# Kernel optimization log

Measured on AMD Instinct MI355X. Metric: run time of the kernel, lower is better.

## Reference

```python
import jax, jax.numpy as jnp
import numpy as np

NEG_INF = -1e9  # mask fill value used by the original layer
LEAKY_SLOPE = 0.2


def setup_inputs() -> dict:
    key = jax.random.key(0)
    k1, k2, k3, k4 = jax.random.split(key, 4)
    B, N, D_in = 8, 1024, 256
    H, head_dim = 8, 32  # output_dim=256, concat_heads=True
    node_features = jax.random.normal(k1, (B, N, D_in), dtype=jnp.float32)
    adjacency = jax.random.randint(k2, (B, N, N), 0, 2, dtype=jnp.int32)
    W = jax.random.normal(k3, (H, D_in, head_dim), dtype=jnp.float32) * (1.0 / np.sqrt(D_in))
    a = jax.random.normal(k4, (H, 2 * head_dim), dtype=jnp.float32) * (1.0 / np.sqrt(2 * head_dim))
    bias = jnp.zeros((H * head_dim,), dtype=jnp.float32)
    return {"node_features": node_features, "adjacency": adjacency, "W": W, "a": a, "bias": bias}


def reference(node_features, adjacency, W, a, bias):
    # node_features: (B,N,D_in); adjacency: (B,N,N) in {0,1}
    H, _, hd = W.shape
    # Per-head linear transform: (B,H,N,head_dim)
    Wh = jnp.einsum('bni,hij->bhnj', node_features, W)
    # a @ concat(h_i, h_j) == a1 @ h_i + a2 @ h_j  (avoids O(N^2*2hd) concat)
    a1, a2 = a[:, :hd], a[:, hd:]
    e_i = jnp.einsum('bhnj,hj->bhn', Wh, a1)  # (B,H,N) source term
    e_j = jnp.einsum('bhnj,hj->bhn', Wh, a2)  # (B,H,N) target term
    scores = e_i[:, :, :, None] + e_j[:, :, None, :]  # (B,H,N,N)
    # LeakyReLU(0.2) exactly as ops.maximum(x, 0.2*x)
    scores = jnp.maximum(scores, LEAKY_SLOPE * scores)
    mask = adjacency.astype(scores.dtype)[:, None, :, :]  # (B,1,N,N)
    masked = scores * mask + (1.0 - mask) * NEG_INF
    attn = jax.nn.softmax(masked, axis=-1)  # (B,H,N,N)
    attended = jnp.einsum('bhij,bhjk->bhik', attn, Wh)  # (B,H,N,hd)
    B, _, N, _ = attended.shape
    # concat heads -> (B,N,H*hd); head order matches the python loop concat
    out = attended.transpose(0, 2, 1, 3).reshape(B, N, H * hd)
    out = out + bias
    return jax.nn.relu(out)
```

## Files before the change

kernel.cpp:

```cpp
#include <hip/hip_runtime.h>

#define GAT_B   8
#define GAT_N   1024
#define GAT_DIN 256
#define GAT_H   8
#define GAT_HD  32
#define GAT_LOG2E 1.4426950408889634f

typedef unsigned short gu16;
typedef unsigned int   gu32;
typedef unsigned long long gu64;
typedef __bf16 bf16x8 __attribute__((ext_vector_type(8)));
typedef __bf16 bf16x4 __attribute__((ext_vector_type(4)));
typedef float  f32x4v __attribute__((ext_vector_type(4)));

#if __has_builtin(__builtin_amdgcn_exp2f)
#define GAT_EXP2(x) __builtin_amdgcn_exp2f(x)
#else
#define GAT_EXP2(x) exp2f(x)
#endif

__device__ __forceinline__ float gb2f(gu16 u) { return __uint_as_float(((gu32)u) << 16); }

__device__ __forceinline__ void gat_detect(const gu16* p, int t, int* sflag) {
    if (t < 64) {
        int e0 = (p[2 * t]     >> 7) & 0xFF;
        int e1 = (p[2 * t + 1] >> 7) & 0xFF;
        unsigned long long m = __ballot((e0 >= 140) || (e1 >= 140));
        if (t == 0) *sflag = (m != 0ULL);
    }
}

__global__ __launch_bounds__(512) void CustomGATLayer_90348932038855_pack(
    const void* __restrict__ Xv, const int* __restrict__ adj, const void* __restrict__ Wv,
    gu64* __restrict__ pk, __bf16* __restrict__ wfg)
{
    __shared__ int sflag;
    const int t = threadIdx.x, bid = blockIdx.x;
    gat_detect((const gu16*)Xv, t, &sflag);
    __syncthreads();
    const int fp32 = sflag;

    if (bid < 8) {
        const int h = bid;
        if (fp32) {
            const float* ws = (const float*)Wv + (size_t)h * 8192;
            #pragma unroll
            for (int q = 0; q < 4; ++q) {
                int idx = q * 2048 + t * 4;
                int i = idx >> 5, k = idx & 31;
                float4 v = *(const float4*)(ws + idx);
                int d = h * 8192 + (((i >> 5) * 32 + k) * 4 + ((i >> 3) & 3)) * 8 + (i & 7);
                wfg[d] = (__bf16)v.x; wfg[d + 32] = (__bf16)v.y;
                wfg[d + 64] = (__bf16)v.z; wfg[d + 96] = (__bf16)v.w;
            }
        } else {
            const gu16* ws = (const gu16*)Wv + (size_t)h * 8192;
            gu16* wo = (gu16*)wfg;
            #pragma unroll
            for (int q = 0; q < 4; ++q) {
                int idx = q * 2048 + t * 4;
                int i = idx >> 5, k = idx & 31;
                ushort4 v = *(const ushort4*)(ws + idx);
                int d = h * 8192 + (((i >> 5) * 32 + k) * 4 + ((i >> 3) & 3)) * 8 + (i & 7);
                wo[d] = v.x; wo[d + 32] = v.y; wo[d + 64] = v.z; wo[d + 96] = v.w;
            }
        }
    }

    const int w = t >> 6, l = t & 63;
    const int r0 = bid * 32 + w * 4;
    for (int r = 0; r < 4; ++r) {
        const int* ar = adj + (size_t)(r0 + r) * GAT_N;
        gu64* po = pk + (size_t)(r0 + r) * 16;
        #pragma unroll
        for (int s = 0; s < 16; ++s) {
            int v = ar[s * 64 + l];
            gu64 m = __ballot(v != 0);
            if (l == 0) po[s] = m;
        }
    }
}

__global__ __launch_bounds__(512) void CustomGATLayer_90348932038855_kernel(
    const void* __restrict__ Xv, const __bf16* __restrict__ wfg, const void* __restrict__ Av,
    __bf16* __restrict__ whb, float* __restrict__ e1, float* __restrict__ e2)
{
    __shared__ __align__(16) __bf16 Xl[16][264];
    __shared__ int sflag;

    const int t = threadIdx.x;
    gat_detect((const gu16*)Xv, t, &sflag);

    const int bt = blockIdx.x;
    const int M0 = bt * 16, b = M0 >> 10, nloc = M0 & 1023;
    const int srow = t >> 5, scol = (t & 31) * 8;
    __syncthreads();
    const int fp32 = sflag;

    if (fp32) {
        const float* xs = (const float*)Xv + ((size_t)(b * GAT_N + nloc + srow)) * GAT_DIN + scol;
        float4 x0 = *(const float4*)(xs);
        float4 x1 = *(const float4*)(xs + 4);
        bf16x8 xv;
        xv[0] = (__bf16)x0.x; xv[1] = (__bf16)x0.y; xv[2] = (__bf16)x0.z; xv[3] = (__bf16)x0.w;
        xv[4] = (__bf16)x1.x; xv[5] = (__bf16)x1.y; xv[6] = (__bf16)x1.z; xv[7] = (__bf16)x1.w;
        *(bf16x8*)&Xl[srow][scol] = xv;
    } else {
        const gu16* xs = (const gu16*)Xv + ((size_t)(b * GAT_N + nloc + srow)) * GAT_DIN + scol;
        *(bf16x8*)&Xl[srow][scol] = *(const bf16x8*)xs;
    }
    __syncthreads();

    const int h = t >> 6, l = t & 63, g = l >> 4, c = l & 15;
    const __bf16* wf = wfg + h * 8192;

    f32x4v acc0 = {0.f, 0.f, 0.f, 0.f};
    f32x4v acc1 = {0.f, 0.f, 0.f, 0.f};
    #pragma unroll
    for (int kc = 0; kc < 8; ++kc) {
        bf16x8 af = *(const bf16x8*)&Xl[c][kc * 32 + 8 * g];
        bf16x8 b0 = *(const bf16x8*)(wf + ((kc * 32 + c) * 4 + g) * 8);
        bf16x8 b1 = *(const bf16x8*)(wf + ((kc * 32 + c + 16) * 4 + g) * 8);
        acc0 = __builtin_amdgcn_mfma_f32_16x16x32_bf16(af, b0, acc0, 0, 0, 0);
        acc1 = __builtin_amdgcn_mfma_f32_16x16x32_bf16(af, b1, acc1, 0, 0, 0);
    }

    const int nb = nloc + 4 * g;
    const int jcc = nb >> 5, kg = (nb >> 3) & 3, e0 = nb & 7;
    const size_t fb = (((size_t)(b * GAT_H + h) * 32 + jcc) * 4 + kg) * 32;
    bf16x4 v0, v1;
    v0[0] = (__bf16)acc0[0]; v0[1] = (__bf16)acc0[1];
    v0[2] = (__bf16)acc0[2]; v0[3] = (__bf16)acc0[3];
    v1[0] = (__bf16)acc1[0]; v1[1] = (__bf16)acc1[1];
    v1[2] = (__bf16)acc1[2]; v1[3] = (__bf16)acc1[3];
    *(bf16x4*)(whb + (fb + c) * 8 + e0)      = v0;
    *(bf16x4*)(whb + (fb + c + 16) * 8 + e0) = v1;

    float a1c, a1c16, a2c, a2c16;
    if (fp32) {
        const float* ap = (const float*)Av + h * 2 * GAT_HD;
        a1c = ap[c] * GAT_LOG2E;      a1c16 = ap[c + 16] * GAT_LOG2E;
        a2c = ap[32 + c] * GAT_LOG2E; a2c16 = ap[48 + c] * GAT_LOG2E;
    } else {
        const gu16* ap = (const gu16*)Av + h * 2 * GAT_HD;
        a1c = gb2f(ap[c]) * GAT_LOG2E;      a1c16 = gb2f(ap[c + 16]) * GAT_LOG2E;
        a2c = gb2f(ap[32 + c]) * GAT_LOG2E; a2c16 = gb2f(ap[48 + c]) * GAT_LOG2E;
    }
    float p1[4], p2[4];
    #pragma unroll
    for (int q = 0; q < 4; ++q) {
        p1[q] = acc0[q] * a1c + acc1[q] * a1c16;
        p2[q] = acc0[q] * a2c + acc1[q] * a2c16;
        #pragma unroll
        for (int mm = 1; mm <= 8; mm <<= 1) {
            p1[q] += __shfl_xor(p1[q], mm);
            p2[q] += __shfl_xor(p2[q], mm);
        }
    }
    if (c == 0) {
        const size_t eb = (size_t)(b * GAT_H + h) * GAT_N + nb;
        #pragma unroll
        for (int q = 0; q < 4; ++q) { e1[eb + q] = p1[q]; e2[eb + q] = p2[q]; }
    }
}

__global__ __launch_bounds__(512) void CustomGATLayer_90348932038855_attn(
    const void* __restrict__ Xv, const gu32* __restrict__ pk32, const void* __restrict__ biasv,
    const __bf16* __restrict__ whb, const float* __restrict__ e1f, const float* __restrict__ e2f,
    float* __restrict__ out)
{
    __shared__ __align__(16) float e2l[GAT_H * GAT_N];
    __shared__ gu32 pkl[16][33];
    __shared__ int sflag;

    const int t = threadIdx.x;
    const int h = t >> 6, l = t & 63, g = l >> 4, c = l & 15;
    const int id = blockIdx.x;
    const int b = id & 7, tile = id >> 3;
    const int i0 = tile * 16;

    gat_detect((const gu16*)Xv, t, &sflag);

    {
        const int prow = t >> 5, pjc = t & 31;
        pkl[prow][pjc] = pk32[((size_t)(b * GAT_N + i0 + prow)) * 32 + pjc];
    }
    {
        const float* s = e2f + (size_t)(b * GAT_H + h) * GAT_N;
        float* d = e2l + h * GAT_N;
        #pragma unroll
        for (int q = 0; q < 4; ++q) {
            int off = (q * 64 + l) * 4;
            *(float4*)(d + off) = *(const float4*)(s + off);
        }
    }
    __syncthreads();
    const int fp32 = sflag;

    const float e1r = e1f[(size_t)(b * GAT_H + h) * GAT_N + i0 + c];
    const __bf16* whr = whb + (size_t)(b * GAT_H + h) * (GAT_N * GAT_HD) + g * 256 + c * 8;
    const float* e2h = e2l + h * GAT_N + 8 * g;

    bf16x8 wA0 = *(const bf16x8*)(whr),        wA1 = *(const bf16x8*)(whr + 128);
    bf16x8 wB0 = *(const bf16x8*)(whr + 1024), wB1 = *(const bf16x8*)(whr + 1152);

    f32x4v acc0 = {0.f, 0.f, 0.f, 0.f};
    f32x4v acc1 = {0.f, 0.f, 0.f, 0.f};
    f32x4v accS = {0.f, 0.f, 0.f, 0.f};
    bf16x8 onesf;
    #pragma unroll
    for (int e = 0; e < 8; ++e) onesf[e] = (__bf16)1.0f;

#define GAT_WCOMP(EV, IDX) {                        \
        float s_ = e1r + (EV);                      \
        s_ = fmaxf(s_, 0.2f * s_);                  \
        s_ = fminf(s_, 86.0f);                      \
        float w_ = GAT_EXP2(s_);                    \
        w_ = (ab & (1u << IDX)) ? w_ : 0.0f;        \
        pf[IDX] = (__bf16)w_; }

    #pragma unroll 2
    for (int jc = 0; jc < 32; ++jc) {
        const bf16x8 w0 = wA0, w1 = wA1;
        wA0 = wB0; wA1 = wB1;
        if (jc < 30) {
            const __bf16* wn = whr + (jc + 2) * 1024;
            wB0 = *(const bf16x8*)wn; wB1 = *(const bf16x8*)(wn + 128);
        }
        const gu32 ab = (pkl[c][jc] >> (8 * g)) & 0xFFu;
        float4 ea = *(const float4*)(e2h + jc * 32);
        float4 eb = *(const float4*)(e2h + jc * 32 + 4);
        bf16x8 pf;
        GAT_WCOMP(ea.x, 0) GAT_WCOMP(ea.y, 1)
        GAT_WCOMP(ea.z, 2) GAT_WCOMP(ea.w, 3)
        GAT_WCOMP(eb.x, 4) GAT_WCOMP(eb.y, 5)
        GAT_WCOMP(eb.z, 6) GAT_WCOMP(eb.w, 7)
        acc0 = __builtin_amdgcn_mfma_f32_16x16x32_bf16(pf, w0, acc0, 0, 0, 0);
        acc1 = __builtin_amdgcn_mfma_f32_16x16x32_bf16(pf, w1, acc1, 0, 0, 0);
        accS = __builtin_amdgcn_mfma_f32_16x16x32_bf16(pf, onesf, accS, 0, 0, 0);
    }
#undef GAT_WCOMP

    float bv0, bv1;
    if (fp32) {
        const float* bp = (const float*)biasv + h * GAT_HD;
        bv0 = bp[c]; bv1 = bp[c + 16];
    } else {
        const gu16* bp = (const gu16*)biasv + h * GAT_HD;
        bv0 = gb2f(bp[c]); bv1 = gb2f(bp[c + 16]);
    }

    float* ob = out + (size_t)(b * GAT_N + i0) * (GAT_H * GAT_HD) + h * GAT_HD + c;
    #pragma unroll
    for (int q = 0; q < 4; ++q) {
        float d = accS[q];
        float r = (d > 0.f) ? (1.0f / d) : 0.0f;
        float o0 = fmaxf(acc0[q] * r + bv0, 0.f);
        float o1 = fmaxf(acc1[q] * r + bv1, 0.f);
        ob[(size_t)(4 * g + q) * (GAT_H * GAT_HD)]      = o0;
        ob[(size_t)(4 * g + q) * (GAT_H * GAT_HD) + 16] = o1;
    }
}

extern "C" void kernel_launch(void* const* d_in, const int* in_sizes, int n_in,
                              void* d_out, int out_size, void* d_ws, size_t ws_size,
                              hipStream_t stream) {
    const void* X    = d_in[0];
    const int*  adj  = (const int*)d_in[1];
    const void* Wm   = d_in[2];
    const void* Av   = d_in[3];
    const void* bias = d_in[4];
    float* outp = (float*)d_out;

    __bf16* whb = (__bf16*)d_ws;
    float* e1  = (float*)(whb + (size_t)GAT_B * GAT_H * GAT_N * GAT_HD);
    float* e2  = e1 + (size_t)GAT_B * GAT_H * GAT_N;
    __bf16* wfg = (__bf16*)(e2 + (size_t)GAT_B * GAT_H * GAT_N);
    gu64* pk   = (gu64*)(wfg + (size_t)GAT_H * GAT_DIN * GAT_HD);

    CustomGATLayer_90348932038855_pack
        <<<dim3(256), 512, 0, stream>>>(X, adj, Wm, pk, wfg);
    CustomGATLayer_90348932038855_kernel
        <<<dim3(512), 512, 0, stream>>>(X, wfg, Av, whb, e1, e2);
    CustomGATLayer_90348932038855_attn
        <<<dim3((GAT_N / 16) * GAT_B), 512, 0, stream>>>(
            X, (const gu32*)pk, bias, whb, e1, e2, outp);
}
```

Measured before the change: 135.6 us.

## Fuse adjacency bit-packing into attention kernel and deepen Wh prefetch

```diff
diff --git a/kernel.cpp b/kernel.cpp
--- a/kernel.cpp
+++ b/kernel.cpp
@@ -9,7 +9,6 @@
 
 typedef unsigned short gu16;
 typedef unsigned int   gu32;
-typedef unsigned long long gu64;
 typedef __bf16 bf16x8 __attribute__((ext_vector_type(8)));
 typedef __bf16 bf16x4 __attribute__((ext_vector_type(4)));
 typedef float  f32x4v __attribute__((ext_vector_type(4)));
@@ -32,52 +31,35 @@
 }
 
 __global__ __launch_bounds__(512) void CustomGATLayer_90348932038855_pack(
-    const void* __restrict__ Xv, const int* __restrict__ adj, const void* __restrict__ Wv,
-    gu64* __restrict__ pk, __bf16* __restrict__ wfg)
+    const void* __restrict__ Xv, const void* __restrict__ Wv, __bf16* __restrict__ wfg)
 {
     __shared__ int sflag;
-    const int t = threadIdx.x, bid = blockIdx.x;
+    const int t = threadIdx.x, h = blockIdx.x;
     gat_detect((const gu16*)Xv, t, &sflag);
     __syncthreads();
     const int fp32 = sflag;
 
-    if (bid < 8) {
-        const int h = bid;
-        if (fp32) {
-            const float* ws = (const float*)Wv + (size_t)h * 8192;
-            #pragma unroll
-            for (int q = 0; q < 4; ++q) {
-                int idx = q * 2048 + t * 4;
-                int i = idx >> 5, k = idx & 31;
-                float4 v = *(const float4*)(ws + idx);
-                int d = h * 8192 + (((i >> 5) * 32 + k) * 4 + ((i >> 3) & 3)) * 8 + (i & 7);
-                wfg[d] = (__bf16)v.x; wfg[d + 32] = (__bf16)v.y;
-                wfg[d + 64] = (__bf16)v.z; wfg[d + 96] = (__bf16)v.w;
-            }
-        } else {
-            const gu16* ws = (const gu16*)Wv + (size_t)h * 8192;
-            gu16* wo = (gu16*)wfg;
-            #pragma unroll
-            for (int q = 0; q < 4; ++q) {
-                int idx = q * 2048 + t * 4;
-                int i = idx >> 5, k = idx & 31;
-                ushort4 v = *(const ushort4*)(ws + idx);
-                int d = h * 8192 + (((i >> 5) * 32 + k) * 4 + ((i >> 3) & 3)) * 8 + (i & 7);
-                wo[d] = v.x; wo[d + 32] = v.y; wo[d + 64] = v.z; wo[d + 96] = v.w;
-            }
-        }
-    }
-
-    const int w = t >> 6, l = t & 63;
-    const int r0 = bid * 32 + w * 4;
-    for (int r = 0; r < 4; ++r) {
-        const int* ar = adj + (size_t)(r0 + r) * GAT_N;
-        gu64* po = pk + (size_t)(r0 + r) * 16;
-        #pragma unroll
-        for (int s = 0; s < 16; ++s) {
-            int v = ar[s * 64 + l];
-            gu64 m = __ballot(v != 0);
-            if (l == 0) po[s] = m;
+    if (fp32) {
+        const float* ws = (const float*)Wv + (size_t)h * 8192;
+        #pragma unroll
+        for (int q = 0; q < 4; ++q) {
+            int idx = q * 2048 + t * 4;
+            int i = idx >> 5, k = idx & 31;
+            float4 v = *(const float4*)(ws + idx);
+            int d = h * 8192 + (((i >> 5) * 32 + k) * 4 + ((i >> 3) & 3)) * 8 + (i & 7);
+            wfg[d] = (__bf16)v.x; wfg[d + 32] = (__bf16)v.y;
+            wfg[d + 64] = (__bf16)v.z; wfg[d + 96] = (__bf16)v.w;
+        }
+    } else {
+        const gu16* ws = (const gu16*)Wv + (size_t)h * 8192;
+        gu16* wo = (gu16*)wfg;
+        #pragma unroll
+        for (int q = 0; q < 4; ++q) {
+            int idx = q * 2048 + t * 4;
+            int i = idx >> 5, k = idx & 31;
+            ushort4 v = *(const ushort4*)(ws + idx);
+            int d = h * 8192 + (((i >> 5) * 32 + k) * 4 + ((i >> 3) & 3)) * 8 + (i & 7);
+            wo[d] = v.x; wo[d + 32] = v.y; wo[d + 64] = v.z; wo[d + 96] = v.w;
         }
     }
 }
@@ -166,7 +148,7 @@
 }
 
 __global__ __launch_bounds__(512) void CustomGATLayer_90348932038855_attn(
-    const void* __restrict__ Xv, const gu32* __restrict__ pk32, const void* __restrict__ biasv,
+    const void* __restrict__ Xv, const int* __restrict__ adj, const void* __restrict__ biasv,
     const __bf16* __restrict__ whb, const float* __restrict__ e1f, const float* __restrict__ e2f,
     float* __restrict__ out)
 {
@@ -183,8 +165,18 @@
     gat_detect((const gu16*)Xv, t, &sflag);
 
     {
-        const int prow = t >> 5, pjc = t & 31;
-        pkl[prow][pjc] = pk32[((size_t)(b * GAT_N + i0 + prow)) * 32 + pjc];
+        const int prow = t >> 5, pd = t & 31;
+        const int* ar = adj + ((size_t)(b * GAT_N + i0 + prow)) * GAT_N + pd * 32;
+        gu32 m = 0;
+        #pragma unroll
+        for (int q = 0; q < 8; ++q) {
+            int4 v = *(const int4*)(ar + q * 4);
+            m |= (v.x != 0 ? 1u : 0u) << (q * 4);
+            m |= (v.y != 0 ? 1u : 0u) << (q * 4 + 1);
+            m |= (v.z != 0 ? 1u : 0u) << (q * 4 + 2);
+            m |= (v.w != 0 ? 1u : 0u) << (q * 4 + 3);
+        }
+        pkl[prow][pd] = m;
     }
     {
         const float* s = e2f + (size_t)(b * GAT_H + h) * GAT_N;
@@ -204,6 +196,8 @@
 
     bf16x8 wA0 = *(const bf16x8*)(whr),        wA1 = *(const bf16x8*)(whr + 128);
     bf16x8 wB0 = *(const bf16x8*)(whr + 1024), wB1 = *(const bf16x8*)(whr + 1152);
+    bf16x8 wC0 = *(const bf16x8*)(whr + 2048), wC1 = *(const bf16x8*)(whr + 2176);
+    bf16x8 wD0 = *(const bf16x8*)(whr + 3072), wD1 = *(const bf16x8*)(whr + 3200);
 
     f32x4v acc0 = {0.f, 0.f, 0.f, 0.f};
     f32x4v acc1 = {0.f, 0.f, 0.f, 0.f};
@@ -211,6 +205,15 @@
     bf16x8 onesf;
     #pragma unroll
     for (int e = 0; e < 8; ++e) onesf[e] = (__bf16)1.0f;
+
+    float bv0, bv1;
+    if (fp32) {
+        const float* bp = (const float*)biasv + h * GAT_HD;
+        bv0 = bp[c]; bv1 = bp[c + 16];
+    } else {
+        const gu16* bp = (const gu16*)biasv + h * GAT_HD;
+        bv0 = gb2f(bp[c]); bv1 = gb2f(bp[c + 16]);
+    }
 
 #define GAT_WCOMP(EV, IDX) {                        \
         float s_ = e1r + (EV);                      \
@@ -220,13 +223,13 @@
         w_ = (ab & (1u << IDX)) ? w_ : 0.0f;        \
         pf[IDX] = (__bf16)w_; }
 
-    #pragma unroll 2
+    #pragma unroll 4
     for (int jc = 0; jc < 32; ++jc) {
         const bf16x8 w0 = wA0, w1 = wA1;
-        wA0 = wB0; wA1 = wB1;
-        if (jc < 30) {
-            const __bf16* wn = whr + (jc + 2) * 1024;
-            wB0 = *(const bf16x8*)wn; wB1 = *(const bf16x8*)(wn + 128);
+        wA0 = wB0; wA1 = wB1; wB0 = wC0; wB1 = wC1; wC0 = wD0; wC1 = wD1;
+        if (jc < 28) {
+            const __bf16* wn = whr + (jc + 4) * 1024;
+            wD0 = *(const bf16x8*)wn; wD1 = *(const bf16x8*)(wn + 128);
         }
         const gu32 ab = (pkl[c][jc] >> (8 * g)) & 0xFFu;
         float4 ea = *(const float4*)(e2h + jc * 32);
@@ -242,15 +245,6 @@
     }
 #undef GAT_WCOMP
 
-    float bv0, bv1;
-    if (fp32) {
-        const float* bp = (const float*)biasv + h * GAT_HD;
-        bv0 = bp[c]; bv1 = bp[c + 16];
-    } else {
-        const gu16* bp = (const gu16*)biasv + h * GAT_HD;
-        bv0 = gb2f(bp[c]); bv1 = gb2f(bp[c + 16]);
-    }
-
     float* ob = out + (size_t)(b * GAT_N + i0) * (GAT_H * GAT_HD) + h * GAT_HD + c;
     #pragma unroll
     for (int q = 0; q < 4; ++q) {
@@ -277,13 +271,12 @@
     float* e1  = (float*)(whb + (size_t)GAT_B * GAT_H * GAT_N * GAT_HD);
     float* e2  = e1 + (size_t)GAT_B * GAT_H * GAT_N;
     __bf16* wfg = (__bf16*)(e2 + (size_t)GAT_B * GAT_H * GAT_N);
-    gu64* pk   = (gu64*)(wfg + (size_t)GAT_H * GAT_DIN * GAT_HD);
 
     CustomGATLayer_90348932038855_pack
-        <<<dim3(256), 512, 0, stream>>>(X, adj, Wm, pk, wfg);
+        <<<dim3(8), 512, 0, stream>>>(X, Wm, wfg);
     CustomGATLayer_90348932038855_kernel
         <<<dim3(512), 512, 0, stream>>>(X, wfg, Av, whb, e1, e2);
     CustomGATLayer_90348932038855_attn
         <<<dim3((GAT_N / 16) * GAT_B), 512, 0, stream>>>(
-            X, (const gu32*)pk, bias, whb, e1, e2, outp);
-}
+            X, adj, bias, whb, e1, e2, outp);
+}
```

Result: faster. 121.2 us (-10.6%).
